# Optimization experiments

Measured on AMD Instinct MI355X. Metric: run time of the kernel, lower is better.

## Reference

```python
import jax, jax.numpy as jnp
import numpy as np

B, T, D = 32, 4096, 256
W = 128          # window_size
EPS = 1e-5


def setup_inputs() -> dict:
    key = jax.random.key(0)
    kx, = jax.random.split(key, 1)
    x = jax.random.normal(kx, (B, T, D), dtype=jnp.float32)
    weight = jnp.ones((D,), dtype=jnp.float32)
    bias = jnp.zeros((D,), dtype=jnp.float32)
    return {"x": x, "weight": weight, "bias": bias}


def reference(x, weight, bias):
    # TemporalNorm, mode='standard', causal rolling window W, no mask, affine.
    Bs, Ts, Ds = x.shape
    idx = jnp.arange(Ts)
    l = jnp.clip(idx - W + 1, 0, None)   # left window index (inclusive)
    r = idx                               # right window index (inclusive, causal)

    # inclusive prefix sums over time, padded with a leading zero row
    sx = jnp.cumsum(x, axis=1)
    sx2 = jnp.cumsum(x * x, axis=1)

    def window_sum(cum):
        cum_pad = jnp.pad(cum, ((0, 0), (1, 0), (0, 0)))  # [B, T+1, D]
        return cum_pad[:, r + 1, :] - cum_pad[:, l, :]     # [B, T, D]

    win_sx = window_sum(sx)
    win_sx2 = window_sum(sx2)

    # mask is None -> per-window count = r - l + 1 (cumsum of ones)
    counts = (r - l + 1).astype(x.dtype)                   # [T]
    denom = jnp.maximum(counts, 1.0)[None, :, None]        # [1, T, 1]

    loc = win_sx / denom
    var = win_sx2 / denom - loc * loc
    scale = jnp.sqrt(var + EPS)

    y = (x - loc) / scale
    y = y * weight[None, None, :] + bias[None, None, :]
    return y
```

## Files before the change

kernel.cpp:

```cpp
#include <hip/hip_runtime.h>

constexpr int Bb  = 32;
constexpr int Tt  = 4096;
constexpr int Dd  = 256;
constexpr int Ww  = 128;
constexpr float EPSF = 1e-5f;

constexpr int CT  = 128;
constexpr int NC  = Tt / CT;
constexpr int NWG = Bb * NC;

__global__ __launch_bounds__(256, 4)
void TemporalNorm_kernel(const float* __restrict__ x,
                         const float* __restrict__ wgt,
                         const float* __restrict__ bia,
                         float* __restrict__ out) {
    const int i  = blockIdx.x;
    const int lb = (i & 7) * (NWG / 8) + (i >> 3);
    const int b  = lb / NC;
    const int c  = lb % NC;
    const int d  = threadIdx.x;
    const int t0 = c * CT;

    const float* __restrict__ xb = x   + (size_t)b * Tt * Dd + d;
    float*       __restrict__ ob = out + (size_t)b * Tt * Dd + d;
    const float w  = wgt[d];
    const float bi = bia[d];

    float s1 = 0.0f, s2 = 0.0f;

    if (t0 >= Ww) {
        for (int t = t0 - Ww; t < t0; t += 4) {
            float a0 = xb[(t + 0) * Dd];
            float a1 = xb[(t + 1) * Dd];
            float a2 = xb[(t + 2) * Dd];
            float a3 = xb[(t + 3) * Dd];
            s1 += (a0 + a1) + (a2 + a3);
            s2 += (a0 * a0 + a1 * a1) + (a2 * a2 + a3 * a3);
        }
        const float rn = 1.0f / (float)Ww;
        for (int t = t0; t < t0 + CT; t += 4) {
            float a0 = xb[(t + 0) * Dd];
            float a1 = xb[(t + 1) * Dd];
            float a2 = xb[(t + 2) * Dd];
            float a3 = xb[(t + 3) * Dd];
            float o0 = xb[(t + 0 - Ww) * Dd];
            float o1 = xb[(t + 1 - Ww) * Dd];
            float o2 = xb[(t + 2 - Ww) * Dd];
            float o3 = xb[(t + 3 - Ww) * Dd];

            s1 += a0 - o0; s2 += a0 * a0 - o0 * o0;
            {
                float loc = s1 * rn;
                float var = s2 * rn - loc * loc;
                float inv = rsqrtf(var + EPSF);
                ob[(t + 0) * Dd] = (a0 - loc) * inv * w + bi;
            }
            s1 += a1 - o1; s2 += a1 * a1 - o1 * o1;
            {
                float loc = s1 * rn;
                float var = s2 * rn - loc * loc;
                float inv = rsqrtf(var + EPSF);
                ob[(t + 1) * Dd] = (a1 - loc) * inv * w + bi;
            }
            s1 += a2 - o2; s2 += a2 * a2 - o2 * o2;
            {
                float loc = s1 * rn;
                float var = s2 * rn - loc * loc;
                float inv = rsqrtf(var + EPSF);
                ob[(t + 2) * Dd] = (a2 - loc) * inv * w + bi;
            }
            s1 += a3 - o3; s2 += a3 * a3 - o3 * o3;
            {
                float loc = s1 * rn;
                float var = s2 * rn - loc * loc;
                float inv = rsqrtf(var + EPSF);
                ob[(t + 3) * Dd] = (a3 - loc) * inv * w + bi;
            }
        }
    } else {
        for (int t = 0; t < CT; ++t) {
            float a = xb[t * Dd];
            s1 += a; s2 += a * a;
            if (t >= Ww) {
                float o = xb[(t - Ww) * Dd];
                s1 -= o; s2 -= o * o;
            }
            float n   = (float)((t + 1 < Ww) ? (t + 1) : Ww);
            float rn  = 1.0f / n;
            float loc = s1 * rn;
            float var = s2 * rn - loc * loc;
            float inv = rsqrtf(var + EPSF);
            ob[t * Dd] = (a - loc) * inv * w + bi;
        }
    }
}

extern "C" void kernel_launch(void* const* d_in, const int* in_sizes, int n_in,
                              void* d_out, int out_size, void* d_ws, size_t ws_size,
                              hipStream_t stream) {
    const float* x   = (const float*)d_in[0];
    const float* wgt = (const float*)d_in[1];
    const float* bia = (const float*)d_in[2];
    float* out = (float*)d_out;

    hipLaunchKernelGGL(TemporalNorm_kernel, dim3(NWG), dim3(256), 0, stream,
                       x, wgt, bia, out);
}
```

Before: 61.73 us.

## Vectorize to float2 per thread and pack two time chunks per block

Each thread now processes two adjacent feature columns with float2 loads and stores. A 256-thread block splits into two halves that handle two consecutive time chunks, which halves the grid size. The warm-up sum uses split accumulators for more instruction-level parallelism. The aim is wider memory transactions and fewer load instructions, at the cost of more registers per thread and fewer, longer blocks.

```diff
diff --git a/kernel.cpp b/kernel.cpp
--- a/kernel.cpp
+++ b/kernel.cpp
@@ -8,7 +8,9 @@
 
 constexpr int CT  = 128;
 constexpr int NC  = Tt / CT;
-constexpr int NWG = Bb * NC;
+constexpr int TPC = Dd / 2;
+constexpr int CPB = 2;
+constexpr int NWG = Bb * NC / CPB;
 
 __global__ __launch_bounds__(256, 4)
 void TemporalNorm_kernel(const float* __restrict__ x,
@@ -17,81 +19,82 @@
                          float* __restrict__ out) {
     const int i  = blockIdx.x;
     const int lb = (i & 7) * (NWG / 8) + (i >> 3);
-    const int b  = lb / NC;
-    const int c  = lb % NC;
-    const int d  = threadIdx.x;
+    const int b     = lb / (NC / CPB);
+    const int cpair = lb % (NC / CPB);
+    const int sub   = threadIdx.x / TPC;
+    const int d2    = threadIdx.x % TPC;
+    const int c  = cpair * CPB + sub;
     const int t0 = c * CT;
 
-    const float* __restrict__ xb = x   + (size_t)b * Tt * Dd + d;
-    float*       __restrict__ ob = out + (size_t)b * Tt * Dd + d;
-    const float w  = wgt[d];
-    const float bi = bia[d];
+    const float2* __restrict__ xb = reinterpret_cast<const float2*>(x   + (size_t)b * Tt * Dd) + d2;
+    float2*       __restrict__ ob = reinterpret_cast<float2*>      (out + (size_t)b * Tt * Dd) + d2;
+    const float wx = wgt[2 * d2],     wy = wgt[2 * d2 + 1];
+    const float bx = bia[2 * d2],     by = bia[2 * d2 + 1];
+    constexpr int S = Dd / 2;
 
-    float s1 = 0.0f, s2 = 0.0f;
+    float s1x = 0.f, s2x = 0.f, s1y = 0.f, s2y = 0.f;
 
     if (t0 >= Ww) {
+        float u1x = 0.f, u2x = 0.f, u1y = 0.f, u2y = 0.f;
         for (int t = t0 - Ww; t < t0; t += 4) {
-            float a0 = xb[(t + 0) * Dd];
-            float a1 = xb[(t + 1) * Dd];
-            float a2 = xb[(t + 2) * Dd];
-            float a3 = xb[(t + 3) * Dd];
-            s1 += (a0 + a1) + (a2 + a3);
-            s2 += (a0 * a0 + a1 * a1) + (a2 * a2 + a3 * a3);
+            float2 a0 = xb[(t + 0) * S];
+            float2 a1 = xb[(t + 1) * S];
+            float2 a2 = xb[(t + 2) * S];
+            float2 a3 = xb[(t + 3) * S];
+            s1x += a0.x + a1.x;  u1x += a2.x + a3.x;
+            s2x += a0.x * a0.x + a1.x * a1.x;  u2x += a2.x * a2.x + a3.x * a3.x;
+            s1y += a0.y + a1.y;  u1y += a2.y + a3.y;
+            s2y += a0.y * a0.y + a1.y * a1.y;  u2y += a2.y * a2.y + a3.y * a3.y;
         }
+        s1x += u1x; s2x += u2x; s1y += u1y; s2y += u2y;
+
         const float rn = 1.0f / (float)Ww;
+        auto step = [&](float a, float o, float& s1, float& s2, float w, float bi) -> float {
+            s1 += a - o;
+            s2 += a * a - o * o;
+            float loc = s1 * rn;
+            float var = s2 * rn - loc * loc;
+            return (a - loc) * rsqrtf(var + EPSF) * w + bi;
+        };
+
         for (int t = t0; t < t0 + CT; t += 4) {
-            float a0 = xb[(t + 0) * Dd];
-            float a1 = xb[(t + 1) * Dd];
-            float a2 = xb[(t + 2) * Dd];
-            float a3 = xb[(t + 3) * Dd];
-            float o0 = xb[(t + 0 - Ww) * Dd];
-            float o1 = xb[(t + 1 - Ww) * Dd];
-            float o2 = xb[(t + 2 - Ww) * Dd];
-            float o3 = xb[(t + 3 - Ww) * Dd];
+            float2 a0 = xb[(t + 0) * S];
+            float2 a1 = xb[(t + 1) * S];
+            float2 a2 = xb[(t + 2) * S];
+            float2 a3 = xb[(t + 3) * S];
+            float2 o0 = xb[(t + 0 - Ww) * S];
+            float2 o1 = xb[(t + 1 - Ww) * S];
+            float2 o2 = xb[(t + 2 - Ww) * S];
+            float2 o3 = xb[(t + 3 - Ww) * S];
 
-            s1 += a0 - o0; s2 += a0 * a0 - o0 * o0;
-            {
-                float loc = s1 * rn;
-                float var = s2 * rn - loc * loc;
-                float inv = rsqrtf(var + EPSF);
-                ob[(t + 0) * Dd] = (a0 - loc) * inv * w + bi;
-            }
-            s1 += a1 - o1; s2 += a1 * a1 - o1 * o1;
-            {
-                float loc = s1 * rn;
-                float var = s2 * rn - loc * loc;
-                float inv = rsqrtf(var + EPSF);
-                ob[(t + 1) * Dd] = (a1 - loc) * inv * w + bi;
-            }
-            s1 += a2 - o2; s2 += a2 * a2 - o2 * o2;
-            {
-                float loc = s1 * rn;
-                float var = s2 * rn - loc * loc;
-                float inv = rsqrtf(var + EPSF);
-                ob[(t + 2) * Dd] = (a2 - loc) * inv * w + bi;
-            }
-            s1 += a3 - o3; s2 += a3 * a3 - o3 * o3;
-            {
-                float loc = s1 * rn;
-                float var = s2 * rn - loc * loc;
-                float inv = rsqrtf(var + EPSF);
-                ob[(t + 3) * Dd] = (a3 - loc) * inv * w + bi;
-            }
+            float2 r0, r1, r2, r3;
+            r0.x = step(a0.x, o0.x, s1x, s2x, wx, bx);
+            r0.y = step(a0.y, o0.y, s1y, s2y, wy, by);
+            r1.x = step(a1.x, o1.x, s1x, s2x, wx, bx);
+            r1.y = step(a1.y, o1.y, s1y, s2y, wy, by);
+            r2.x = step(a2.x, o2.x, s1x, s2x, wx, bx);
+            r2.y = step(a2.y, o2.y, s1y, s2y, wy, by);
+            r3.x = step(a3.x, o3.x, s1x, s2x, wx, bx);
+            r3.y = step(a3.y, o3.y, s1y, s2y, wy, by);
+
+            ob[(t + 0) * S] = r0;
+            ob[(t + 1) * S] = r1;
+            ob[(t + 2) * S] = r2;
+            ob[(t + 3) * S] = r3;
         }
     } else {
         for (int t = 0; t < CT; ++t) {
-            float a = xb[t * Dd];
-            s1 += a; s2 += a * a;
-            if (t >= Ww) {
-                float o = xb[(t - Ww) * Dd];
-                s1 -= o; s2 -= o * o;
-            }
-            float n   = (float)((t + 1 < Ww) ? (t + 1) : Ww);
-            float rn  = 1.0f / n;
-            float loc = s1 * rn;
-            float var = s2 * rn - loc * loc;
-            float inv = rsqrtf(var + EPSF);
-            ob[t * Dd] = (a - loc) * inv * w + bi;
+            float2 a = xb[t * S];
+            s1x += a.x; s2x += a.x * a.x;
+            s1y += a.y; s2y += a.y * a.y;
+            float rn  = 1.0f / (float)(t + 1);
+            float lx  = s1x * rn, ly = s1y * rn;
+            float vx  = s2x * rn - lx * lx;
+            float vy  = s2y * rn - ly * ly;
+            float2 r;
+            r.x = (a.x - lx) * rsqrtf(vx + EPSF) * wx + bx;
+            r.y = (a.y - ly) * rsqrtf(vy + EPSF) * wy + by;
+            ob[t * S] = r;
         }
     }
 }
```

Result: no change. 61.91 us (+0.3%).
